# Kernel tuning notes

Measured on AMD Instinct MI355X. Metric: run time of the kernel, lower is better.

The kernel has to match this reference:

```python
import jax, jax.numpy as jnp
import numpy as np

N = 50000      # nodes
E = 800000     # edges (before self loops)
IN = 128       # in_channels
HID = 32       # hidden_channels per head
HEADS = 4
NC = 10        # num_classes
NEG_SLOPE = 0.2  # PyG GATConv default


def setup_inputs() -> dict:
    key = jax.random.key(0)
    ks = jax.random.split(key, 11)
    g = lambda k, shape, fan: (jax.random.normal(k, shape, jnp.float32) / np.float32(np.sqrt(fan)))
    return {
        "x": jax.random.normal(ks[0], (N, IN), jnp.float32),
        "edge_index": jax.random.randint(ks[1], (2, E), 0, N, dtype=jnp.int64),
        # layer 1: GATConv(IN -> HID, heads=HEADS, concat=True)
        "W1": g(ks[2], (IN, HEADS * HID), IN),
        "att_src1": g(ks[3], (HEADS, HID), HID),
        "att_dst1": g(ks[4], (HEADS, HID), HID),
        "b1": jnp.zeros((HEADS * HID,), jnp.float32),
        # layer 2: GATConv(HEADS*HID -> NC, heads=1, concat=False)
        "W2": g(ks[5], (HEADS * HID, NC), HEADS * HID),
        "att_src2": g(ks[6], (1, NC), NC),
        "att_dst2": g(ks[7], (1, NC), NC),
        "b2": jnp.zeros((NC,), jnp.float32),
    }


def gat_conv(x, edge_index, W, att_src, att_dst, bias, heads, out_ch, concat):
    n = x.shape[0]
    # add self loops (PyG GATConv default add_self_loops=True)
    loop = jnp.arange(n, dtype=edge_index.dtype)
    src = jnp.concatenate([edge_index[0], loop])  # message sources j
    dst = jnp.concatenate([edge_index[1], loop])  # message targets i
    h = (x @ W).reshape(n, heads, out_ch)          # [N,H,C]
    a_s = jnp.sum(h * att_src, axis=-1)            # [N,H]
    a_d = jnp.sum(h * att_dst, axis=-1)            # [N,H]
    e = jax.nn.leaky_relu(a_s[src] + a_d[dst], NEG_SLOPE)  # [Etot,H]
    # segment softmax over incoming edges of each target node
    m = jax.ops.segment_max(e, dst, num_segments=n)        # [N,H]
    ex = jnp.exp(e - m[dst])
    denom = jax.ops.segment_sum(ex, dst, num_segments=n)   # [N,H]
    alpha = ex / denom[dst]                                 # [Etot,H]
    # weighted scatter-aggregate of source features
    out = jax.ops.segment_sum(h[src] * alpha[:, :, None], dst, num_segments=n)  # [N,H,C]
    out = out.reshape(n, heads * out_ch) if concat else out.mean(axis=1)
    return out + bias


def reference(x, edge_index, W1, att_src1, att_dst1, b1, W2, att_src2, att_dst2, b2):
    h = gat_conv(x, edge_index, W1, att_src1, att_dst1, b1, HEADS, HID, True)
    h = jax.nn.elu(h)
    # dropout(p=0.5, training=self.training): identity in eval mode
    return gat_conv(h, edge_index, W2, att_src2, att_dst2, b2, 1, NC, False)
```

## Files before the change

### kernel.cpp

```cpp
#include <hip/hip_runtime.h>
#include <hip/hip_fp16.h>
#include <math.h>

#define NN 50000
#define NE 800000
#define INC 128
#define NHEAD 4
#define NCLS 10
#define NSLOPE 0.2f
#define CAP 48
#define NGRP (NN / 16)
#define BW 512
#define NBUK 98
#define BSTRIDE 10752
#define CHUNK 3125

typedef _Float16 f16x8 __attribute__((ext_vector_type(8)));
typedef float f32x4 __attribute__((ext_vector_type(4)));

__device__ __forceinline__ float lrelu(float e) { return fmaxf(e, NSLOPE * e); }

__global__ void k_wtz(const float* __restrict__ W1, __half* __restrict__ wt,
                      int* __restrict__ bcnt) {
    const int idx = blockIdx.x * 256 + threadIdx.x;
    const int c = idx >> 7, k = idx & 127;
    wt[c * 128 + (k ^ ((c & 7) << 3))] = __float2half(W1[k * 128 + c]);
    if (idx < 128) bcnt[idx] = 0;
}

__global__ __launch_bounds__(256) void k_p1(const int* __restrict__ ei,
                                            int* __restrict__ bcnt,
                                            unsigned* __restrict__ bbuf) {
    __shared__ unsigned stage[CHUNK];
    __shared__ int lcnt[NBUK], lbase[NBUK];
    const int tid = threadIdx.x;
    const int e0 = blockIdx.x * CHUNK;
    if (tid < NBUK) lcnt[tid] = 0;
    __syncthreads();
    for (int k = tid; k < CHUNK; k += 256) {
        const int i = e0 + k;
        const int d = ei[NE + i];
        const int s = ei[i];
        const int b = d >> 9;
        stage[k] = (unsigned)s | ((unsigned)(d & 511) << 16) | ((unsigned)b << 25);
        atomicAdd(&lcnt[b], 1);
    }
    __syncthreads();
    if (tid < NBUK) {
        lbase[tid] = atomicAdd(&bcnt[tid], lcnt[tid]);
        lcnt[tid] = 0;
    }
    __syncthreads();
    for (int k = tid; k < CHUNK; k += 256) {
        const unsigned pk = stage[k];
        const int b = pk >> 25;
        const int slot = atomicAdd(&lcnt[b], 1);
        const int pos = lbase[b] + slot;
        if (pos < BSTRIDE) bbuf[(size_t)b * BSTRIDE + pos] = pk;
    }
}

__global__ __launch_bounds__(256) void k_p2(const int* __restrict__ bcnt,
                                            const unsigned* __restrict__ bbuf,
                                            unsigned short* __restrict__ ell,
                                            int* __restrict__ cnt) {
    __shared__ __align__(16) unsigned short lell[BW * CAP];
    __shared__ int lc[BW];
    const int b = blockIdx.x;
    const int tid = threadIdx.x;
    const int base_d = b * BW;
    const int nd = min(BW, NN - base_d);
    lc[tid] = 0; lc[tid + 256] = 0;
    __syncthreads();
    const int m = min(bcnt[b], BSTRIDE);
    for (int i = tid; i < m; i += 256) {
        const unsigned pk = bbuf[(size_t)b * BSTRIDE + i];
        const int dl = (pk >> 16) & 511;
        const int c = atomicAdd(&lc[dl], 1);
        if (c < CAP) lell[dl * CAP + c] = (unsigned short)(pk & 0xFFFFu);
    }
    __syncthreads();
    const int nq = nd * 6;
    uint4* dstp = (uint4*)(ell + (size_t)base_d * CAP);
    const uint4* srcp = (const uint4*)lell;
    for (int j = tid; j < nq; j += 256) dstp[j] = srcp[j];
    for (int j = tid; j < nd; j += 256) cnt[base_d + j] = lc[j];
}

__global__ __launch_bounds__(256) void k_gemm1(
        const float* __restrict__ x, const __half* __restrict__ wt,
        const float* __restrict__ atts, const float* __restrict__ attd,
        __half* __restrict__ h1, float* __restrict__ a_s, float* __restrict__ a_d) {
    const int tid = threadIdx.x;
    const int w = tid >> 6, lane = tid & 63;
    const int l15 = lane & 15, l4 = lane >> 4;
    __shared__ __align__(16) __half xh[16 * 128];
    f16x8 af[2][4];
    float atA[2][4], adA[2][4];
    #pragma unroll
    for (int t = 0; t < 2; ++t) {
        const int c = w * 32 + t * 16 + l15;
        #pragma unroll
        for (int ks = 0; ks < 4; ++ks) {
            const int kh = (ks * 32 + l4 * 8) ^ ((c & 7) << 3);
            af[t][ks] = *(const f16x8*)&wt[c * 128 + kh];
        }
        #pragma unroll
        for (int r = 0; r < 4; ++r) {
            const int cc = w * 32 + t * 16 + l4 * 4 + r;
            atA[t][r] = atts[cc];
            adA[t][r] = attd[cc];
        }
    }
    const int srow = tid >> 4, sk0 = (tid & 15) * 8;
    const unsigned swb = ((unsigned)(srow & 7)) << 4;
    const int n0 = blockIdx.x * 16;
    {
        float4 xa = *(const float4*)&x[(size_t)(n0 + srow) * INC + sk0];
        float4 xb = *(const float4*)&x[(size_t)(n0 + srow) * INC + sk0 + 4];
        __half2 c0 = __floats2half2_rn(xa.x, xa.y);
        __half2 c1 = __floats2half2_rn(xa.z, xa.w);
        __half2 c2 = __floats2half2_rn(xb.x, xb.y);
        __half2 c3 = __floats2half2_rn(xb.z, xb.w);
        uint4 st;
        st.x = *(unsigned*)&c0; st.y = *(unsigned*)&c1;
        st.z = *(unsigned*)&c2; st.w = *(unsigned*)&c3;
        *(uint4*)((char*)xh + (srow * 256 + ((sk0 * 2) ^ swb))) = st;
    }
    __syncthreads();
    f32x4 acc0 = {0.f, 0.f, 0.f, 0.f}, acc1 = {0.f, 0.f, 0.f, 0.f};
    #pragma unroll
    for (int ks = 0; ks < 4; ++ks) {
        const int kb = (ks * 64 + l4 * 16) ^ ((l15 & 7) << 4);
        f16x8 bf = *(const f16x8*)((const char*)xh + (l15 * 256 + kb));
        acc0 = __builtin_amdgcn_mfma_f32_16x16x32_f16(af[0][ks], bf, acc0, 0, 0, 0);
        acc1 = __builtin_amdgcn_mfma_f32_16x16x32_f16(af[1][ks], bf, acc1, 0, 0, 0);
    }
    const int nrow = n0 + l15;
    {
        __half2 p0 = __floats2half2_rn(acc0[0], acc0[1]);
        __half2 p1 = __floats2half2_rn(acc0[2], acc0[3]);
        uint2 st; st.x = *(unsigned*)&p0; st.y = *(unsigned*)&p1;
        *(uint2*)&h1[(size_t)nrow * INC + w * 32 + l4 * 4] = st;
        __half2 q0 = __floats2half2_rn(acc1[0], acc1[1]);
        __half2 q1 = __floats2half2_rn(acc1[2], acc1[3]);
        uint2 su; su.x = *(unsigned*)&q0; su.y = *(unsigned*)&q1;
        *(uint2*)&h1[(size_t)nrow * INC + w * 32 + 16 + l4 * 4] = su;
    }
    float vs = acc0[0]*atA[0][0] + acc0[1]*atA[0][1] + acc0[2]*atA[0][2] + acc0[3]*atA[0][3]
             + acc1[0]*atA[1][0] + acc1[1]*atA[1][1] + acc1[2]*atA[1][2] + acc1[3]*atA[1][3];
    float vd = acc0[0]*adA[0][0] + acc0[1]*adA[0][1] + acc0[2]*adA[0][2] + acc0[3]*adA[0][3]
             + acc1[0]*adA[1][0] + acc1[1]*adA[1][1] + acc1[2]*adA[1][2] + acc1[3]*adA[1][3];
    vs += __shfl_xor(vs, 16, 64); vs += __shfl_xor(vs, 32, 64);
    vd += __shfl_xor(vd, 16, 64); vd += __shfl_xor(vd, 32, 64);
    if (lane < 16) {
        a_s[(n0 + lane) * NHEAD + w] = vs;
        a_d[(n0 + lane) * NHEAD + w] = vd;
    }
}

#define WPB 4
__global__ __launch_bounds__(256) void k_agg1(
        const int* __restrict__ cnt, const unsigned short* __restrict__ ell,
        const float* __restrict__ a_s, const float* __restrict__ a_d,
        const __half* __restrict__ h1, const float* __restrict__ b1,
        __half* __restrict__ helu) {
    const int wid = threadIdx.x >> 6;
    const int lane = threadIdx.x & 63;
    const int n = blockIdx.x * WPB + wid;
    __shared__ float4 pl[WPB][64];
    const int cn = min(cnt[n], CAP);
    const size_t base = (size_t)n * CAP;
    const int c8 = lane & 15, slot = lane >> 4;
    const int hg = c8 >> 2;
    const float4 adv = *(const float4*)&a_d[n * 4];
    const float advh = hg == 0 ? adv.x : hg == 1 ? adv.y : hg == 2 ? adv.z : adv.w;
    const float psv = __expf(lrelu(a_s[n * 4 + hg] + advh));
    int s_reg = 0;
    float4 p4 = make_float4(0.f, 0.f, 0.f, 0.f);
    if (lane < cn) {
        s_reg = ell[base + lane];
        float4 av = *(const float4*)&a_s[s_reg * 4];
        p4.x = __expf(lrelu(av.x + adv.x));
        p4.y = __expf(lrelu(av.y + adv.y));
        p4.z = __expf(lrelu(av.z + adv.z));
        p4.w = __expf(lrelu(av.w + adv.w));
    }
    pl[wid][lane] = p4;
    __syncthreads();
    const float* plw = (const float*)&pl[wid][0];
    __half2 ha[4], hb[4];
    #pragma unroll
    for (int k = 0; k < 4; ++k) {
        ha[k] = __float2half2_rn(0.f);
        hb[k] = __float2half2_rn(0.f);
    }
    float den = 0.f;
    const int iters = (cn + 7) >> 3;
    for (int t = 0; t < iters; ++t) {
        const int iA = t * 8 + slot, iB = iA + 4;
        const int sA = __shfl(s_reg, iA, 64);
        const int sB = __shfl(s_reg, iB, 64);
        const float pA = plw[iA * 4 + hg];
        const float pB = plw[iB * 4 + hg];
        den += pA + pB;
        uint4 vA = *(const uint4*)(h1 + (__umul24(sA, INC) + c8 * 8));
        uint4 vB = *(const uint4*)(h1 + (__umul24(sB, INC) + c8 * 8));
        const __half2 pA2 = __float2half2_rn(pA);
        const __half2 pB2 = __float2half2_rn(pB);
        ha[0] = __hfma2(pA2, *(__half2*)&vA.x, ha[0]);
        ha[1] = __hfma2(pA2, *(__half2*)&vA.y, ha[1]);
        ha[2] = __hfma2(pA2, *(__half2*)&vA.z, ha[2]);
        ha[3] = __hfma2(pA2, *(__half2*)&vA.w, ha[3]);
        hb[0] = __hfma2(pB2, *(__half2*)&vB.x, hb[0]);
        hb[1] = __hfma2(pB2, *(__half2*)&vB.y, hb[1]);
        hb[2] = __hfma2(pB2, *(__half2*)&vB.z, hb[2]);
        hb[3] = __hfma2(pB2, *(__half2*)&vB.w, hb[3]);
    }
    float acc[8];
    #pragma unroll
    for (int k = 0; k < 4; ++k) {
        float2 fa = __half22float2(ha[k]);
        float2 fb = __half22float2(hb[k]);
        acc[2 * k]     = fa.x + fb.x;
        acc[2 * k + 1] = fa.y + fb.y;
    }
    #pragma unroll
    for (int k = 0; k < 8; ++k) {
        acc[k] += __shfl_xor(acc[k], 16, 64);
        acc[k] += __shfl_xor(acc[k], 32, 64);
    }
    den += __shfl_xor(den, 16, 64);
    den += __shfl_xor(den, 32, 64);
    if (slot == 0) {
        const float psum = den + psv;
        uint4 v = *(const uint4*)(h1 + (__umul24(n, INC) + c8 * 8));
        float2 f;
        f = __half22float2(*(__half2*)&v.x); acc[0]=fmaf(psv,f.x,acc[0]); acc[1]=fmaf(psv,f.y,acc[1]);
        f = __half22float2(*(__half2*)&v.y); acc[2]=fmaf(psv,f.x,acc[2]); acc[3]=fmaf(psv,f.y,acc[3]);
        f = __half22float2(*(__half2*)&v.z); acc[4]=fmaf(psv,f.x,acc[4]); acc[5]=fmaf(psv,f.y,acc[5]);
        f = __half22float2(*(__half2*)&v.w); acc[6]=fmaf(psv,f.x,acc[6]); acc[7]=fmaf(psv,f.y,acc[7]);
        const float inv = 1.f / psum;
        float4 b0 = *(const float4*)&b1[c8 * 8];
        float4 b4 = *(const float4*)&b1[c8 * 8 + 4];
        const float bb[8] = {b0.x, b0.y, b0.z, b0.w, b4.x, b4.y, b4.z, b4.w};
        float o[8];
        #pragma unroll
        for (int k = 0; k < 8; ++k) {
            float t = fmaf(acc[k], inv, bb[k]);
            o[k] = t > 0.f ? t : expm1f(t);
        }
        __half2 o0 = __floats2half2_rn(o[0], o[1]);
        __half2 o1 = __floats2half2_rn(o[2], o[3]);
        __half2 o2 = __floats2half2_rn(o[4], o[5]);
        __half2 o3 = __floats2half2_rn(o[6], o[7]);
        uint4 st;
        st.x = *(unsigned*)&o0; st.y = *(unsigned*)&o1;
        st.z = *(unsigned*)&o2; st.w = *(unsigned*)&o3;
        *(uint4*)&helu[(size_t)n * INC + c8 * 8] = st;
    }
}

__global__ void k_gemm2(const __half* __restrict__ helu, const float* __restrict__ W2,
                        const float* __restrict__ atts, const float* __restrict__ attd,
                        float* __restrict__ h2, float* __restrict__ a_s2,
                        float* __restrict__ a_d2) {
    __shared__ float Ws[INC * NCLS];
    const int tid = threadIdx.x;
    for (int i = tid; i < INC * NCLS; i += blockDim.x) Ws[i] = W2[i];
    __syncthreads();
    const int n = blockIdx.x * blockDim.x + tid;
    if (n >= NN) return;
    float acc[NCLS];
    #pragma unroll
    for (int c = 0; c < NCLS; ++c) acc[c] = 0.f;
    for (int k8 = 0; k8 < INC; k8 += 8) {
        uint4 q = *(const uint4*)&helu[(size_t)n * INC + k8];
        float2 f01 = __half22float2(*(__half2*)&q.x);
        float2 f23 = __half22float2(*(__half2*)&q.y);
        float2 f45 = __half22float2(*(__half2*)&q.z);
        float2 f67 = __half22float2(*(__half2*)&q.w);
        float xv[8] = {f01.x, f01.y, f23.x, f23.y, f45.x, f45.y, f67.x, f67.y};
        #pragma unroll
        for (int u = 0; u < 8; ++u) {
            #pragma unroll
            for (int c = 0; c < NCLS; ++c)
                acc[c] = fmaf(xv[u], Ws[(k8 + u) * NCLS + c], acc[c]);
        }
    }
    float vs = 0.f, vd = 0.f;
    #pragma unroll
    for (int c = 0; c < NCLS; ++c) {
        h2[(size_t)n * NCLS + c] = acc[c];
        vs += acc[c] * atts[c];
        vd += acc[c] * attd[c];
    }
    a_s2[n] = vs;
    a_d2[n] = vd;
}

__global__ __launch_bounds__(256) void k_agg2(
        const int* __restrict__ cnt, const unsigned short* __restrict__ ell,
        const float* __restrict__ a_s2, const float* __restrict__ a_d2,
        const float* __restrict__ h2, const float* __restrict__ b2,
        float* __restrict__ outp) {
    const int wid = threadIdx.x >> 6;
    const int lane = threadIdx.x & 63;
    const int n = blockIdx.x * WPB + wid;
    const int cn = min(cnt[n], CAP);
    const size_t base = (size_t)n * CAP;
    const float adv = a_d2[n];
    const float pself = __expf(lrelu(a_s2[n] + adv));
    float p = 0.f; int s_reg = 0;
    if (lane < cn) {
        s_reg = ell[base + lane];
        p = __expf(lrelu(a_s2[s_reg] + adv));
    }
    float q = p;
    #pragma unroll
    for (int off = 1; off < 64; off <<= 1) q += __shfl_xor(q, off, 64);
    const float psum = q + pself;
    const int slot = lane >> 4, ch = lane & 15;
    const int chv = (ch < NCLS) ? ch : 0;
    float acc = 0.f;
    const int iters = (cn + 3) >> 2;
    for (int t = 0; t < iters; ++t) {
        const int i = t * 4 + slot;
        const int s_i = __shfl(s_reg, i, 64);
        const float p_i = __shfl(p, i, 64);
        acc = fmaf(p_i, h2[__umul24(s_i, NCLS) + chv], acc);
    }
    acc += __shfl_xor(acc, 16, 64);
    acc += __shfl_xor(acc, 32, 64);
    if (lane < NCLS)
        outp[(size_t)n * NCLS + lane] =
            fmaf(pself, h2[__umul24(n, NCLS) + lane], acc) / psum + b2[lane];
}

extern "C" void kernel_launch(void* const* d_in, const int* in_sizes, int n_in,
                              void* d_out, int out_size, void* d_ws, size_t ws_size,
                              hipStream_t stream) {
    const float* x    = (const float*)d_in[0];
    const int*   ei   = (const int*)d_in[1];
    const float* W1   = (const float*)d_in[2];
    const float* as1w = (const float*)d_in[3];
    const float* ad1w = (const float*)d_in[4];
    const float* b1   = (const float*)d_in[5];
    const float* W2   = (const float*)d_in[6];
    const float* as2w = (const float*)d_in[7];
    const float* ad2w = (const float*)d_in[8];
    const float* b2   = (const float*)d_in[9];
    float* out = (float*)d_out;

    float* wsf  = (float*)d_ws;
    __half* h1  = (__half*)wsf;
    float* as1  = wsf + (size_t)NN * 64;
    float* ad1  = as1 + (size_t)NN * NHEAD;
    int*   cnt  = (int*)(ad1 + (size_t)NN * NHEAD);
    unsigned short* ell = (unsigned short*)(cnt + NN);
    __half* helu = (__half*)((float*)(cnt + NN) + (size_t)NN * 24);
    __half* wt  = (__half*)((float*)helu + (size_t)NN * 64);
    int*   bcnt = (int*)(wt + 16384);
    unsigned* bbuf = (unsigned*)(bcnt + 128);
    float* h2   = wsf;
    float* as2  = wsf + (size_t)NN * NCLS;
    float* ad2  = as2 + NN;

    k_wtz<<<64, 256, 0, stream>>>(W1, wt, bcnt);
    k_p1<<<256, 256, 0, stream>>>(ei, bcnt, bbuf);
    k_p2<<<NBUK, 256, 0, stream>>>(bcnt, bbuf, ell, cnt);
    k_gemm1<<<NGRP, 256, 0, stream>>>(x, wt, as1w, ad1w, h1, as1, ad1);
    k_agg1<<<NN / WPB, 256, 0, stream>>>(cnt, ell, as1, ad1, h1, b1, helu);
    k_gemm2<<<(NN + 255) / 256, 256, 0, stream>>>(helu, W2, as2w, ad2w, h2, as2, ad2);
    k_agg2<<<NN / WPB, 256, 0, stream>>>(cnt, ell, as2, ad2, h2, b2, out);
}
```

Baseline: 119.7 us.

## Fuse layer-2 projection and attention logits into layer-1 aggregation kernel

```diff
diff --git a/kernel.cpp b/kernel.cpp
--- a/kernel.cpp
+++ b/kernel.cpp
@@ -164,11 +164,18 @@
         const int* __restrict__ cnt, const unsigned short* __restrict__ ell,
         const float* __restrict__ a_s, const float* __restrict__ a_d,
         const __half* __restrict__ h1, const float* __restrict__ b1,
-        __half* __restrict__ helu) {
+        const float* __restrict__ W2, const float* __restrict__ atts2,
+        const float* __restrict__ attd2, float* __restrict__ h2o,
+        float* __restrict__ as2, float* __restrict__ ad2) {
     const int wid = threadIdx.x >> 6;
     const int lane = threadIdx.x & 63;
     const int n = blockIdx.x * WPB + wid;
     __shared__ float4 pl[WPB][64];
+    __shared__ float W2s[NCLS * INC];
+    for (int i = threadIdx.x; i < NCLS * INC; i += 256) {
+        const int c = i >> 7, k = i & 127;
+        W2s[c * 128 + k] = W2[k * NCLS + c];
+    }
     const int cn = min(cnt[n], CAP);
     const size_t base = (size_t)n * CAP;
     const int c8 = lane & 15, slot = lane >> 4;
@@ -248,55 +255,34 @@
         #pragma unroll
         for (int k = 0; k < 8; ++k) {
             float t = fmaf(acc[k], inv, bb[k]);
-            o[k] = t > 0.f ? t : expm1f(t);
-        }
-        __half2 o0 = __floats2half2_rn(o[0], o[1]);
-        __half2 o1 = __floats2half2_rn(o[2], o[3]);
-        __half2 o2 = __floats2half2_rn(o[4], o[5]);
-        __half2 o3 = __floats2half2_rn(o[6], o[7]);
-        uint4 st;
-        st.x = *(unsigned*)&o0; st.y = *(unsigned*)&o1;
-        st.z = *(unsigned*)&o2; st.w = *(unsigned*)&o3;
-        *(uint4*)&helu[(size_t)n * INC + c8 * 8] = st;
-    }
-}
-
-__global__ void k_gemm2(const __half* __restrict__ helu, const float* __restrict__ W2,
-                        const float* __restrict__ atts, const float* __restrict__ attd,
-                        float* __restrict__ h2, float* __restrict__ a_s2,
-                        float* __restrict__ a_d2) {
-    __shared__ float Ws[INC * NCLS];
-    const int tid = threadIdx.x;
-    for (int i = tid; i < INC * NCLS; i += blockDim.x) Ws[i] = W2[i];
-    __syncthreads();
-    const int n = blockIdx.x * blockDim.x + tid;
-    if (n >= NN) return;
-    float acc[NCLS];
-    #pragma unroll
-    for (int c = 0; c < NCLS; ++c) acc[c] = 0.f;
-    for (int k8 = 0; k8 < INC; k8 += 8) {
-        uint4 q = *(const uint4*)&helu[(size_t)n * INC + k8];
-        float2 f01 = __half22float2(*(__half2*)&q.x);
-        float2 f23 = __half22float2(*(__half2*)&q.y);
-        float2 f45 = __half22float2(*(__half2*)&q.z);
-        float2 f67 = __half22float2(*(__half2*)&q.w);
-        float xv[8] = {f01.x, f01.y, f23.x, f23.y, f45.x, f45.y, f67.x, f67.y};
-        #pragma unroll
-        for (int u = 0; u < 8; ++u) {
+            o[k] = t > 0.f ? t : (__expf(t) - 1.0f);
+        }
+        float h2p[NCLS];
+        #pragma unroll
+        for (int c = 0; c < NCLS; ++c) {
+            float s = 0.f;
             #pragma unroll
-            for (int c = 0; c < NCLS; ++c)
-                acc[c] = fmaf(xv[u], Ws[(k8 + u) * NCLS + c], acc[c]);
-        }
-    }
-    float vs = 0.f, vd = 0.f;
-    #pragma unroll
-    for (int c = 0; c < NCLS; ++c) {
-        h2[(size_t)n * NCLS + c] = acc[c];
-        vs += acc[c] * atts[c];
-        vd += acc[c] * attd[c];
-    }
-    a_s2[n] = vs;
-    a_d2[n] = vd;
+            for (int k = 0; k < 8; ++k)
+                s = fmaf(o[k], W2s[c * 128 + c8 * 8 + k], s);
+            h2p[c] = s;
+        }
+        #pragma unroll
+        for (int c = 0; c < NCLS; ++c) {
+            h2p[c] += __shfl_xor(h2p[c], 1, 16);
+            h2p[c] += __shfl_xor(h2p[c], 2, 16);
+            h2p[c] += __shfl_xor(h2p[c], 4, 16);
+            h2p[c] += __shfl_xor(h2p[c], 8, 16);
+        }
+        float vs2 = 0.f, vd2 = 0.f, myh2 = 0.f;
+        #pragma unroll
+        for (int c = 0; c < NCLS; ++c) {
+            vs2 = fmaf(h2p[c], atts2[c], vs2);
+            vd2 = fmaf(h2p[c], attd2[c], vd2);
+            myh2 = (c8 == c) ? h2p[c] : myh2;
+        }
+        if (c8 < NCLS) h2o[__umul24(n, NCLS) + c8] = myh2;
+        if (c8 == 0) { as2[n] = vs2; ad2[n] = vd2; }
+    }
 }
 
 __global__ __launch_bounds__(256) void k_agg2(
@@ -358,19 +344,18 @@
     float* ad1  = as1 + (size_t)NN * NHEAD;
     int*   cnt  = (int*)(ad1 + (size_t)NN * NHEAD);
     unsigned short* ell = (unsigned short*)(cnt + NN);
-    __half* helu = (__half*)((float*)(cnt + NN) + (size_t)NN * 24);
-    __half* wt  = (__half*)((float*)helu + (size_t)NN * 64);
+    float* h2   = (float*)(cnt + NN) + (size_t)NN * 24;
+    float* as2  = h2 + (size_t)NN * NCLS;
+    float* ad2  = as2 + NN;
+    __half* wt  = (__half*)(ad2 + NN);
     int*   bcnt = (int*)(wt + 16384);
     unsigned* bbuf = (unsigned*)(bcnt + 128);
-    float* h2   = wsf;
-    float* as2  = wsf + (size_t)NN * NCLS;
-    float* ad2  = as2 + NN;
 
     k_wtz<<<64, 256, 0, stream>>>(W1, wt, bcnt);
     k_p1<<<256, 256, 0, stream>>>(ei, bcnt, bbuf);
     k_p2<<<NBUK, 256, 0, stream>>>(bcnt, bbuf, ell, cnt);
     k_gemm1<<<NGRP, 256, 0, stream>>>(x, wt, as1w, ad1w, h1, as1, ad1);
-    k_agg1<<<NN / WPB, 256, 0, stream>>>(cnt, ell, as1, ad1, h1, b1, helu);
-    k_gemm2<<<(NN + 255) / 256, 256, 0, stream>>>(helu, W2, as2w, ad2w, h2, as2, ad2);
+    k_agg1<<<NN / WPB, 256, 0, stream>>>(cnt, ell, as1, ad1, h1, b1,
+                                         W2, as2w, ad2w, h2, as2, ad2);
     k_agg2<<<NN / WPB, 256, 0, stream>>>(cnt, ell, as2, ad2, h2, b2, out);
 }
```

Result: slower. 125.9 us (+5.3%).
